# Kernel optimization log

Measured on AMD Instinct MI355X. Metric: run time of the kernel, lower is better.

The kernel has to match this reference:

```python
import jax, jax.numpy as jnp
import numpy as np

PATCH = 24  # self.current_patch
STRIDE = PATCH // 2


def _conv(x, w, b):
    # NCHW conv, SAME padding, stride 1 (= Conv2d(k=3, padding=1))
    y = jax.lax.conv_general_dilated(x, w, (1, 1), 'SAME',
                                     dimension_numbers=('NCHW', 'OIHW', 'NCHW'))
    return y + b[None, :, None, None]


def setup_inputs() -> dict:
    key = jax.random.key(0)
    ks = jax.random.split(key, 9)
    b, c, h, w = 2, 64, 192, 192
    s = 0.05  # keep sigmoid/tanh unsaturated
    return {
        'source': jax.random.normal(ks[0], (b, c, h, w), jnp.float32),
        'target': jax.random.normal(ks[1], (b, c, h, w), jnp.float32),
        # deform_net params (128->512->256->1)
        'W1': jax.random.normal(ks[2], (512, 128, 3, 3), jnp.float32) * s,
        'b1': jnp.zeros((512,), jnp.float32),
        'W2': jax.random.normal(ks[3], (256, 512, 3, 3), jnp.float32) * s,
        'b2': jnp.zeros((256,), jnp.float32),
        'W3': jax.random.normal(ks[4], (1, 256, 3, 3), jnp.float32) * s,
        'b3': jnp.zeros((1,), jnp.float32),
        # reg_net params (128->512->64->1); original declared 256 in-ch (bug), fixed to 128
        'Wr1': jax.random.normal(ks[5], (512, 128, 3, 3), jnp.float32) * s,
        'br1': jnp.zeros((512,), jnp.float32),
        'Wr2': jax.random.normal(ks[6], (64, 512, 3, 3), jnp.float32) * s,
        'br2': jnp.zeros((64,), jnp.float32),
        'Wr3': jax.random.normal(ks[7], (1, 64, 3, 3), jnp.float32) * s,
        'br3': jnp.zeros((1,), jnp.float32),
    }


def _attention(src, tgt, W1, b1, W2, b2, W3, b3):
    b, c, h, w = src.shape
    p, st = PATCH, STRIDE
    nH = (h - p) // st + 1
    nW = (w - p) // st + 1
    # patch gather indices
    r_idx = jnp.arange(nH)[:, None] * st + jnp.arange(p)[None, :]  # [nH, p]
    c_idx = jnp.arange(nW)[:, None] * st + jnp.arange(p)[None, :]  # [nW, p]
    # [b, c, nH, nW, p, p]
    def gather(x):
        return x[:, :, r_idx[:, None, :, None], c_idx[None, :, None, :]]
    ps = gather(src)
    pt = gather(tgt)
    # -> [b*nH*nW, 2c, p, p]  (one big batched conv replaces the python loop)
    pair = jnp.concatenate([ps, pt], axis=1)            # [b, 2c, nH, nW, p, p]
    pair = pair.transpose(0, 2, 3, 1, 4, 5).reshape(b * nH * nW, 2 * c, p, p)
    x = jax.nn.relu(_conv(pair, W1, b1))
    x = jax.nn.relu(_conv(x, W2, b2))
    score = jax.nn.sigmoid(_conv(x, W3, b3))            # [b*nH*nW, 1, p, p]
    score = score.reshape(b, nH, nW, 1, p, p).transpose(0, 3, 1, 2, 4, 5)  # [b,1,nH,nW,p,p]
    # overlap-add scatter (duplicate indices accumulate)
    R = jnp.broadcast_to(r_idx[:, None, :, None], (nH, nW, p, p))
    C = jnp.broadcast_to(c_idx[None, :, None, :], (nH, nW, p, p))
    att = jnp.zeros((b, 1, h, w), src.dtype).at[:, :, R, C].add(score)
    cnt = jnp.zeros((b, 1, h, w), src.dtype).at[:, :, R, C].add(1.0)
    return att / jnp.maximum(cnt, 1.0)


def reference(source, target, W1, b1, W2, b2, W3, b3, Wr1, br1, Wr2, br2, Wr3, br3):
    attention_map = _attention(source, target, W1, b1, W2, b2, W3, b3)
    x = jnp.concatenate([source, target], axis=1)       # [b, 128, h, w]
    x = jax.nn.relu(_conv(x, Wr1, br1))
    x = jax.nn.relu(_conv(x, Wr2, br2))
    registered = jnp.tanh(_conv(x, Wr3, br3))           # [b, 1, h, w]
    return registered, attention_map
```

## Files before the change

kernel.cpp:

```cpp
#include <hip/hip_runtime.h>
#include <cmath>

typedef _Float16 half8  __attribute__((ext_vector_type(8)));
typedef _Float16 half4v __attribute__((ext_vector_type(4)));
typedef float    float4v __attribute__((ext_vector_type(4)));

template<int MT, int NT, int MODE>
__global__ __launch_bounds__(256, 2)
void mfma_conv(const _Float16* __restrict__ in, const _Float16* __restrict__ Wg,
               const float* __restrict__ bias, _Float16* __restrict__ out,
               int CI, int CO, int RSin, int RSout, int NB, int NC, int p0)
{
    constexpr int CHUNKS_PH = 3 * MT * 64;
    constexpr int STAGE_N   = CHUNKS_PH / 256;
    __shared__ __align__(16) _Float16 sW[2][CHUNKS_PH * 8];

    const int tid  = threadIdx.x;
    const int wave = tid >> 6;
    const int lane = tid & 63;
    const int ll   = lane & 15;
    const int quad = lane >> 4;

    const int NSUB = NC * (9 / NT);
    const int id   = blockIdx.x;
    const int xcd  = id & 7;
    const int slot = id >> 3;
    const int unit = (slot / NSUB) * 8 + xcd;
    const int rem  = slot % NSUB;
    const int pxb  = rem / NC;
    const int co_t = rem % NC;
    if (unit >= NB) return;
    const int co0 = co_t * (MT * 16);
    const int pbase = pxb * (NT * 64) + wave * (NT * 16);

    size_t in_base, out_base;
    int TY = 0, TX = 0;
    int b_off[NT], edge[NT];
    if (MODE == 0) {
        int pat = p0 + unit;
        int bb = pat / 225, remp = pat % 225;
        int pi = remp / 15, pj = remp % 15;
        in_base  = (size_t)bb * RSin * RSin * CI;
        out_base = (size_t)unit * 676 * CO;
        #pragma unroll
        for (int nt = 0; nt < NT; ++nt) {
            int p = pbase + nt * 16 + ll;
            int py = p / 24, px = p % 24;
            b_off[nt] = ((pi * 12 + py) * RSin + (pj * 12 + px)) * CI;
            edge[nt] = (py == 0 ? 1 : 0) | (py == 23 ? 2 : 0)
                     | (px == 0 ? 4 : 0) | (px == 23 ? 8 : 0);
        }
    } else if (MODE == 1) {
        in_base  = (size_t)unit * 676 * CI;
        out_base = (size_t)unit * 676 * CO;
        #pragma unroll
        for (int nt = 0; nt < NT; ++nt) {
            int p = pbase + nt * 16 + ll;
            b_off[nt] = ((p / 24) * RSin + (p % 24)) * CI;
            edge[nt] = 0;
        }
    } else {
        int tile = unit & 63, b = unit >> 6;
        TY = (tile >> 3) * 24; TX = (tile & 7) * 24;
        in_base  = (size_t)b * RSin * RSin * CI;
        out_base = (size_t)b * RSout * RSout * CO;
        #pragma unroll
        for (int nt = 0; nt < NT; ++nt) {
            int p = pbase + nt * 16 + ll;
            b_off[nt] = ((TY + p / 24) * RSin + (TX + p % 24)) * CI;
            edge[nt] = 0;
        }
    }

    auto stage = [&](int buf, int ci0, int dy) {
        #pragma unroll
        for (int k = 0; k < STAGE_N; ++k) {
            int c = tid + k * 256;
            int lane_s = c & 63;
            int mtt = c >> 6;
            int mt = mtt % MT, dxl = mtt / MT;
            const _Float16* src =
                &Wg[((size_t)(co0 + mt * 16 + (lane_s & 15)) * 9 + (dy * 3 + dxl)) * CI
                    + ci0 + (lane_s >> 4) * 8];
            __builtin_amdgcn_global_load_lds(
                (const __attribute__((address_space(1))) void*)src,
                (__attribute__((address_space(3))) void*)&sW[buf][(size_t)c * 8],
                16, 0, 0);
        }
    };

    float4v acc[MT][NT];
    #pragma unroll
    for (int mt = 0; mt < MT; ++mt)
        #pragma unroll
        for (int nt = 0; nt < NT; ++nt)
            acc[mt][nt] = (float4v){0.f, 0.f, 0.f, 0.f};

    const int phases = (CI >> 5) * 3;
    stage(0, 0, 0);

    int buf = 0, ci0 = 0, dy = 0;
    for (int ph = 0; ph < phases; ++ph) {
        const int dy_n = (dy == 2) ? 0 : dy + 1;
        const int ci_n = (dy == 2) ? ci0 + 32 : ci0;
        if (ph + 1 < phases) {
            stage(buf ^ 1, ci_n, dy_n);
            if (MT == 8) asm volatile("s_waitcnt vmcnt(6)" ::: "memory");
            else         asm volatile("s_waitcnt vmcnt(3)" ::: "memory");
        } else {
            asm volatile("s_waitcnt vmcnt(0)" ::: "memory");
        }
        __builtin_amdgcn_s_barrier();
        __builtin_amdgcn_sched_barrier(0);

        __builtin_amdgcn_s_setprio(1);
        const _Float16* inp = in + in_base + ci0 + quad * 8;
        const int rowoff = dy * RSin * CI;
        #pragma unroll
        for (int dx = 0; dx < 3; ++dx) {
            const int toff = rowoff + dx * CI;
            const int emask = (dy == 0 ? 1 : 0) | (dy == 2 ? 2 : 0)
                            | (dx == 0 ? 4 : 0) | (dx == 2 ? 8 : 0);
            half8 a[MT];
            #pragma unroll
            for (int mt = 0; mt < MT; ++mt)
                a[mt] = *(const half8*)&sW[buf][((dx * MT + mt) * 64 + lane) * 8];
            #pragma unroll
            for (int nt = 0; nt < NT; ++nt) {
                uint4 raw = *(const uint4*)(inp + b_off[nt] + toff);
                if (MODE == 0) {
                    bool z = (edge[nt] & emask) != 0;
                    raw.x = z ? 0u : raw.x;
                    raw.y = z ? 0u : raw.y;
                    raw.z = z ? 0u : raw.z;
                    raw.w = z ? 0u : raw.w;
                }
                half8 b = *(half8*)&raw;
                #pragma unroll
                for (int mt = 0; mt < MT; ++mt)
                    acc[mt][nt] = __builtin_amdgcn_mfma_f32_16x16x32_f16(
                        a[mt], b, acc[mt][nt], 0, 0, 0);
            }
        }
        __builtin_amdgcn_s_setprio(0);
        asm volatile("" ::: "memory");
        __builtin_amdgcn_s_barrier();
        buf ^= 1; dy = dy_n; ci0 = ci_n;
    }

    #pragma unroll
    for (int mt = 0; mt < MT; ++mt) {
        float4v bs = *(const float4v*)&bias[co0 + mt * 16 + quad * 4];
        #pragma unroll
        for (int nt = 0; nt < NT; ++nt) {
            int p = pbase + nt * 16 + ll;
            size_t ooff = out_base
                + (size_t)((TY + p / 24 + 1) * RSout + (TX + p % 24) + 1) * CO
                + co0 + mt * 16 + quad * 4;
            float4v v = acc[mt][nt];
            half4v h;
            h.x = (_Float16)fmaxf(v.x + bs.x, 0.f);
            h.y = (_Float16)fmaxf(v.y + bs.y, 0.f);
            h.z = (_Float16)fmaxf(v.z + bs.z, 0.f);
            h.w = (_Float16)fmaxf(v.w + bs.w, 0.f);
            *(half4v*)(out + ooff) = h;
        }
    }
}

static inline int swiz_grid(int NB, int NC, int PXB) {
    return ((NB + 7) & ~7) * NC * PXB;
}

template<int MODE, int ACT, int NT>
__global__ __launch_bounds__(256, 2)
void mfma_score(const _Float16* __restrict__ in, const _Float16* __restrict__ W16,
                const float* __restrict__ bias, float* __restrict__ outp,
                int CI, int RSI, int NB, int PXB)
{
    __shared__ __align__(16) _Float16 sW[9 * 16 * 32];

    const int tid  = threadIdx.x;
    const int wave = tid >> 6;
    const int lane = tid & 63;
    const int ll   = lane & 15;
    const int quad = lane >> 4;

    const int unit = blockIdx.x / PXB;
    const int pxb  = blockIdx.x % PXB;
    if (unit >= NB) return;
    const int pbase = pxb * (NT * 64) + wave * (NT * 16);

    size_t in_base;
    int ty = 0, tx = 0, bb = 0;
    if (MODE == 2) {
        bb = unit >> 6; int tile = unit & 63; ty = (tile >> 3) * 24; tx = (tile & 7) * 24;
        in_base = (size_t)bb * RSI * RSI * CI;
    } else {
        in_base = (size_t)unit * 676 * CI;
    }

    int b_off[NT];
    #pragma unroll
    for (int nt = 0; nt < NT; ++nt) {
        int p = pbase + nt * 16 + ll;
        b_off[nt] = ((ty + p / 24) * RSI + (tx + p % 24)) * CI;
    }

    float4v acc[NT];
    #pragma unroll
    for (int nt = 0; nt < NT; ++nt) acc[nt] = (float4v){0.f, 0.f, 0.f, 0.f};

    for (int ci0 = 0; ci0 < CI; ci0 += 32) {
        __syncthreads();
        for (int c = tid; c < 9 * 16 * 4; c += 256) {
            int q = c & 3, tco = c >> 2;
            int t = tco >> 4, co = tco & 15;
            *(uint4*)&sW[tco * 32 + q * 8] =
                *(const uint4*)&W16[((size_t)co * 9 + t) * CI + ci0 + q * 8];
        }
        __syncthreads();

        const _Float16* inp = in + in_base + ci0 + quad * 8;
        for (int dy = 0; dy < 3; ++dy)
            for (int dx = 0; dx < 3; ++dx) {
                const int t = dy * 3 + dx;
                const int toff = (dy * RSI + dx) * CI;
                half8 a = *(const half8*)&sW[(t * 16 + ll) * 32 + quad * 8];
                #pragma unroll
                for (int nt = 0; nt < NT; ++nt) {
                    half8 b = *(const half8*)(inp + b_off[nt] + toff);
                    acc[nt] = __builtin_amdgcn_mfma_f32_16x16x32_f16(a, b, acc[nt], 0, 0, 0);
                }
            }
    }

    if (quad == 0) {
        float bv = bias[0];
        #pragma unroll
        for (int nt = 0; nt < NT; ++nt) {
            int p = pbase + nt * 16 + ll;
            float v = acc[nt].x + bv;
            if (ACT == 1) {
                outp[(size_t)unit * 576 + p] = 1.f / (1.f + expf(-v));
            } else {
                int y = ty + p / 24, x = tx + p % 24;
                outp[(size_t)bb * 36864 + y * 192 + x] = tanhf(v);
            }
        }
    }
}

__global__ __launch_bounds__(256)
void build_x16i(const float* __restrict__ src, const float* __restrict__ tgt,
                _Float16* __restrict__ X)
{
    int idx = blockIdx.x * 256 + threadIdx.x;
    int q = idx & 15, pid = idx >> 4;
    if (pid >= 2 * 36864) return;
    int b = pid / 36864, r = pid % 36864;
    int y = r / 192, x = r % 192;
    half8 h;
    #pragma unroll
    for (int j = 0; j < 8; ++j) {
        int ch = q * 8 + j;
        const float* im = (ch < 64) ? src : tgt;
        h[j] = (_Float16)im[(size_t)(b * 64 + (ch & 63)) * 36864 + r];
    }
    *(half8*)&X[(((size_t)b * 194 + y + 1) * 194 + (x + 1)) * 128 + q * 8] = h;
}

__global__ __launch_bounds__(256)
void cvt_w(const float* __restrict__ src, _Float16* __restrict__ dst, int CO, int CI)
{
    int idx = blockIdx.x * 256 + threadIdx.x;
    if (idx >= CO * 9 * CI) return;
    int ci = idx % CI, t = (idx / CI) % 9, co = idx / (9 * CI);
    dst[idx] = (_Float16)src[((size_t)co * CI + ci) * 9 + t];
}

__global__ __launch_bounds__(256)
void cvt_pad16(const float* __restrict__ src, _Float16* __restrict__ dst, int CI)
{
    int idx = blockIdx.x * 256 + threadIdx.x;
    if (idx >= 16 * 9 * CI) return;
    int ci = idx % CI, t = (idx / CI) % 9, co = idx / (9 * CI);
    dst[idx] = (co == 0) ? (_Float16)src[(size_t)ci * 9 + t] : (_Float16)0.0f;
}

__global__ __launch_bounds__(256)
void ring_zero(_Float16* __restrict__ buf, int npatch, int RS, int CI)
{
    int c8 = CI >> 3;
    int RC = 2 * RS + 2 * (RS - 2);
    int idx = blockIdx.x * 256 + threadIdx.x;
    if (idx >= npatch * RC * c8) return;
    int q = idx % c8, rp = (idx / c8) % RC, pl = idx / (c8 * RC);
    int r, c;
    if (rp < RS)            { r = 0;      c = rp; }
    else if (rp < 2 * RS)   { r = RS - 1; c = rp - RS; }
    else {
        int s = rp - 2 * RS, half = RS - 2;
        if (s < half) { r = s + 1;        c = 0; }
        else          { r = s - half + 1; c = RS - 1; }
    }
    uint4 z = {0u, 0u, 0u, 0u};
    *(uint4*)&buf[((size_t)pl * RS * RS + r * RS + c) * CI + q * 8] = z;
}

__global__ __launch_bounds__(256)
void att_finalize(const float* __restrict__ score, float* __restrict__ out)
{
    int idx = blockIdx.x * 256 + threadIdx.x;
    if (idx >= 2 * 36864) return;
    int b = idx / 36864, r = idx % 36864;
    int y = r / 192, x = r % 192;
    int i_lo = (y >= 24) ? (y - 12) / 12 : 0;
    int i_hi = min(14, y / 12);
    int j_lo = (x >= 24) ? (x - 12) / 12 : 0;
    int j_hi = min(14, x / 12);
    float s = 0.f; int cnt = 0;
    for (int i = i_lo; i <= i_hi; ++i)
        for (int j = j_lo; j <= j_hi; ++j) {
            s += score[(((size_t)b * 15 + i) * 15 + j) * 576 + (y - 12 * i) * 24 + (x - 12 * j)];
            ++cnt;
        }
    out[idx] = s / (float)cnt;
}

extern "C" void kernel_launch(void* const* d_in, const int* in_sizes, int n_in,
                              void* d_out, int out_size, void* d_ws, size_t ws_size,
                              hipStream_t stream)
{
    const float* src = (const float*)d_in[0];
    const float* tgt = (const float*)d_in[1];
    const float* W1  = (const float*)d_in[2];  const float* b1  = (const float*)d_in[3];
    const float* W2  = (const float*)d_in[4];  const float* b2  = (const float*)d_in[5];
    const float* W3  = (const float*)d_in[6];  const float* b3  = (const float*)d_in[7];
    const float* Wr1 = (const float*)d_in[8];  const float* br1 = (const float*)d_in[9];
    const float* Wr2 = (const float*)d_in[10]; const float* br2 = (const float*)d_in[11];
    const float* Wr3 = (const float*)d_in[12]; const float* br3 = (const float*)d_in[13];
    float* out = (float*)d_out;

    _Float16* ws = (_Float16*)d_ws;
    size_t o = 0;
    _Float16* X16i = ws + o; o += (size_t)2 * 194 * 194 * 128;
    _Float16* W1h  = ws + o; o += (size_t)512 * 9 * 128;
    _Float16* W2h  = ws + o; o += (size_t)256 * 9 * 512;
    _Float16* Wr1h = ws + o; o += (size_t)512 * 9 * 128;
    _Float16* Wr2h = ws + o; o += (size_t)64 * 9 * 512;
    _Float16* W3p  = ws + o; o += (size_t)16 * 9 * 256;
    _Float16* Wr3p = ws + o; o += (size_t)16 * 9 * 64;
    float*    score = (float*)(ws + o); o += 2 * 259200;
    const size_t fixed_h = o;

    const size_t per_patch_h = (size_t)676 * (512 + 256);
    const size_t regA_h = (size_t)2 * 194 * 194 * 512;
    const size_t regB_h = (size_t)2 * 194 * 194 * 64;
    size_t h_avail = ws_size / 2;
    int P = 50;
    {
        size_t n450 = 450 * per_patch_h; if (n450 < regA_h + regB_h) n450 = regA_h + regB_h;
        size_t n150 = 150 * per_patch_h; if (n150 < regA_h + regB_h) n150 = regA_h + regB_h;
        if (h_avail >= fixed_h + n450)      P = 450;
        else if (h_avail >= fixed_h + n150) P = 150;
    }
    const int nchunks = 450 / P;

    _Float16* D1 = ws + fixed_h;
    _Float16* D2 = D1 + (size_t)P * 676 * 512;

    ring_zero<<<(2 * 772 * 16 + 255) / 256, 256, 0, stream>>>(X16i, 2, 194, 128);
    build_x16i<<<4608, 256, 0, stream>>>(src, tgt, X16i);
    cvt_w<<<2304, 256, 0, stream>>>(W1,  W1h,  512, 128);
    cvt_w<<<4608, 256, 0, stream>>>(W2,  W2h,  256, 512);
    cvt_w<<<2304, 256, 0, stream>>>(Wr1, Wr1h, 512, 128);
    cvt_w<<<1152, 256, 0, stream>>>(Wr2, Wr2h, 64,  512);
    cvt_pad16<<<(16 * 9 * 256 + 255) / 256, 256, 0, stream>>>(W3,  W3p,  256);
    cvt_pad16<<<(16 * 9 * 64  + 255) / 256, 256, 0, stream>>>(Wr3, Wr3p, 64);

    ring_zero<<<(P * 100 * 64 + 255) / 256, 256, 0, stream>>>(D1, P, 26, 512);
    ring_zero<<<(P * 100 * 32 + 255) / 256, 256, 0, stream>>>(D2, P, 26, 256);
    for (int c = 0; c < nchunks; ++c) {
        int p0 = c * P;
        mfma_conv<8, 3, 0><<<swiz_grid(P, 4, 3), 256, 0, stream>>>(
            X16i, W1h, b1, D1, 128, 512, 194, 26, P, 4, p0);
        mfma_conv<8, 3, 1><<<swiz_grid(P, 2, 3), 256, 0, stream>>>(
            D1, W2h, b2, D2, 512, 256, 26, 26, P, 2, 0);
        mfma_score<1, 1, 3><<<P * 3, 256, 0, stream>>>(
            D2, W3p, b3, score + (size_t)p0 * 576, 256, 26, P, 3);
    }
    att_finalize<<<288, 256, 0, stream>>>(score, out + 73728);

    {
        _Float16* A1 = ws + fixed_h;
        _Float16* A2 = A1 + ((P >= 150) ? regA_h : (size_t)194 * 194 * 512);
        if (P >= 150) {
            ring_zero<<<(2 * 772 * 64 + 255) / 256, 256, 0, stream>>>(A1, 2, 194, 512);
            ring_zero<<<(2 * 772 * 8  + 255) / 256, 256, 0, stream>>>(A2, 2, 194, 64);
            mfma_conv<8, 3, 2><<<swiz_grid(128, 4, 3), 256, 0, stream>>>(
                X16i, Wr1h, br1, A1, 128, 512, 194, 194, 128, 4, 0);
            mfma_conv<4, 3, 2><<<swiz_grid(128, 1, 3), 256, 0, stream>>>(
                A1, Wr2h, br2, A2, 512, 64, 194, 194, 128, 1, 0);
            mfma_score<2, 2, 3><<<128 * 3, 256, 0, stream>>>(
                A2, Wr3p, br3, out, 64, 194, 128, 3);
        } else {
            for (int b = 0; b < 2; ++b) {
                ring_zero<<<(772 * 64 + 255) / 256, 256, 0, stream>>>(A1, 1, 194, 512);
                ring_zero<<<(772 * 8  + 255) / 256, 256, 0, stream>>>(A2, 1, 194, 64);
                mfma_conv<8, 3, 2><<<swiz_grid(64, 4, 3), 256, 0, stream>>>(
                    X16i + (size_t)b * 194 * 194 * 128, Wr1h, br1, A1,
                    128, 512, 194, 194, 64, 4, 0);
                mfma_conv<4, 3, 2><<<swiz_grid(64, 1, 3), 256, 0, stream>>>(
                    A1, Wr2h, br2, A2, 512, 64, 194, 194, 64, 1, 0);
                mfma_score<2, 2, 3><<<64 * 3, 256, 0, stream>>>(
                    A2, Wr3p, br3, out + (size_t)b * 36864, 64, 194, 64, 3);
            }
        }
    }
}
```

Baseline: 2.211 ms.

## Triple-buffer weight staging and prefetch activation loads one phase ahead

Moves the conv kernel's weight staging from double to triple LDS buffering, so stage loads are issued two phases ahead. Activation (B operand) global loads are now issued into registers one phase early, alternating between two register sets. Fine-grained vmcnt waits replace the old per-phase full stall, and one barrier per phase replaces two. The goal is to hide global-memory latency behind MFMA work, at the cost of more LDS and VGPR use, which may lower occupancy or cause spills under launch_bounds(256,2).

```diff
diff --git a/kernel.cpp b/kernel.cpp
--- a/kernel.cpp
+++ b/kernel.cpp
@@ -4,6 +4,13 @@
 typedef _Float16 half8  __attribute__((ext_vector_type(8)));
 typedef _Float16 half4v __attribute__((ext_vector_type(4)));
 typedef float    float4v __attribute__((ext_vector_type(4)));
+
+template<int N> __device__ __forceinline__ void vwait() {
+    if constexpr      (N == 15) asm volatile("s_waitcnt vmcnt(15)" ::: "memory");
+    else if constexpr (N == 12) asm volatile("s_waitcnt vmcnt(12)" ::: "memory");
+    else if constexpr (N == 9)  asm volatile("s_waitcnt vmcnt(9)"  ::: "memory");
+    else                        asm volatile("s_waitcnt vmcnt(0)"  ::: "memory");
+}
 
 template<int MT, int NT, int MODE>
 __global__ __launch_bounds__(256, 2)
@@ -13,7 +20,8 @@
 {
     constexpr int CHUNKS_PH = 3 * MT * 64;
     constexpr int STAGE_N   = CHUNKS_PH / 256;
-    __shared__ __align__(16) _Float16 sW[2][CHUNKS_PH * 8];
+    constexpr int VF        = STAGE_N + 9;
+    __shared__ __align__(16) _Float16 sW[3][CHUNKS_PH * 8];
 
     const int tid  = threadIdx.x;
     const int wave = tid >> 6;
@@ -72,7 +80,7 @@
         }
     }
 
-    auto stage = [&](int buf, int ci0, int dy) {
+    auto stage = [&](int bufI, int ci0, int dy) {
         #pragma unroll
         for (int k = 0; k < STAGE_N; ++k) {
             int c = tid + k * 256;
@@ -84,9 +92,19 @@
                     + ci0 + (lane_s >> 4) * 8];
             __builtin_amdgcn_global_load_lds(
                 (const __attribute__((address_space(1))) void*)src,
-                (__attribute__((address_space(3))) void*)&sW[buf][(size_t)c * 8],
+                (__attribute__((address_space(3))) void*)&sW[bufI][(size_t)c * 8],
                 16, 0, 0);
         }
+    };
+
+    auto bload = [&](uint4 (&B)[NT][3], int ci0, int dy) {
+        const _Float16* inp = in + in_base + ci0 + quad * 8;
+        const int rowoff = dy * RSin * CI;
+        #pragma unroll
+        for (int nt = 0; nt < NT; ++nt)
+            #pragma unroll
+            for (int dx = 0; dx < 3; ++dx)
+                B[nt][dx] = *(const uint4*)(inp + b_off[nt] + rowoff + dx * CI);
     };
 
     float4v acc[MT][NT];
@@ -96,38 +114,18 @@
         for (int nt = 0; nt < NT; ++nt)
             acc[mt][nt] = (float4v){0.f, 0.f, 0.f, 0.f};
 
-    const int phases = (CI >> 5) * 3;
-    stage(0, 0, 0);
-
-    int buf = 0, ci0 = 0, dy = 0;
-    for (int ph = 0; ph < phases; ++ph) {
-        const int dy_n = (dy == 2) ? 0 : dy + 1;
-        const int ci_n = (dy == 2) ? ci0 + 32 : ci0;
-        if (ph + 1 < phases) {
-            stage(buf ^ 1, ci_n, dy_n);
-            if (MT == 8) asm volatile("s_waitcnt vmcnt(6)" ::: "memory");
-            else         asm volatile("s_waitcnt vmcnt(3)" ::: "memory");
-        } else {
-            asm volatile("s_waitcnt vmcnt(0)" ::: "memory");
-        }
-        __builtin_amdgcn_s_barrier();
-        __builtin_amdgcn_sched_barrier(0);
-
-        __builtin_amdgcn_s_setprio(1);
-        const _Float16* inp = in + in_base + ci0 + quad * 8;
-        const int rowoff = dy * RSin * CI;
+    auto compute = [&](int bufI, uint4 (&B)[NT][3], int dy) {
         #pragma unroll
         for (int dx = 0; dx < 3; ++dx) {
-            const int toff = rowoff + dx * CI;
             const int emask = (dy == 0 ? 1 : 0) | (dy == 2 ? 2 : 0)
                             | (dx == 0 ? 4 : 0) | (dx == 2 ? 8 : 0);
             half8 a[MT];
             #pragma unroll
             for (int mt = 0; mt < MT; ++mt)
-                a[mt] = *(const half8*)&sW[buf][((dx * MT + mt) * 64 + lane) * 8];
+                a[mt] = *(const half8*)&sW[bufI][((dx * MT + mt) * 64 + lane) * 8];
             #pragma unroll
             for (int nt = 0; nt < NT; ++nt) {
-                uint4 raw = *(const uint4*)(inp + b_off[nt] + toff);
+                uint4 raw = B[nt][dx];
                 if (MODE == 0) {
                     bool z = (edge[nt] & emask) != 0;
                     raw.x = z ? 0u : raw.x;
@@ -142,11 +140,46 @@
                         a[mt], b, acc[mt][nt], 0, 0, 0);
             }
         }
-        __builtin_amdgcn_s_setprio(0);
-        asm volatile("" ::: "memory");
-        __builtin_amdgcn_s_barrier();
-        buf ^= 1; dy = dy_n; ci0 = ci_n;
-    }
+    };
+
+    uint4 bA[NT][3], bB[NT][3];
+
+    const int phases = (CI >> 5) * 3;
+    stage(0, 0, 0);
+    stage(1, 0, 1);
+    bload(bA, 0, 0);
+
+    int bufC = 0, dyC = 0, ciC = 0;
+    int bufS = 2, dyS = 2, ciS = 0;
+    int dyB = 1, ciB = 0;
+
+#define ADV(dy, ci) do { if (dy == 2) { dy = 0; ci += 32; } else ++dy; } while (0)
+#define PH(BCUR, BNXT, HASS, HASB, VN)                                      \
+    do {                                                                    \
+        __builtin_amdgcn_s_barrier();                                       \
+        if (HASS) { stage(bufS, ciS, dyS);                                  \
+                    bufS = (bufS == 2) ? 0 : bufS + 1; ADV(dyS, ciS); }     \
+        if (HASB) { bload(BNXT, ciB, dyB); ADV(dyB, ciB); }                 \
+        vwait<VN>();                                                        \
+        __builtin_amdgcn_sched_barrier(0);                                  \
+        __builtin_amdgcn_s_setprio(1);                                      \
+        compute(bufC, BCUR, dyC);                                           \
+        __builtin_amdgcn_s_setprio(0);                                      \
+        bufC = (bufC == 2) ? 0 : bufC + 1; ADV(dyC, ciC);                   \
+    } while (0)
+
+    for (int it = 0; it < (phases - 6) / 2; ++it) {
+        PH(bA, bB, 1, 1, VF);
+        PH(bB, bA, 1, 1, VF);
+    }
+    PH(bA, bB, 1, 1, VF);
+    PH(bB, bA, 1, 1, VF);
+    PH(bA, bB, 1, 1, VF);
+    PH(bB, bA, 1, 1, VF);
+    PH(bA, bB, 0, 1, 9);
+    PH(bB, bA, 0, 0, 0);
+#undef PH
+#undef ADV
 
     #pragma unroll
     for (int mt = 0; mt < MT; ++mt) {
```

Result: no change. 2.217 ms (+0.3%).
